# Performance work log

Hardware: AMD Instinct MI355X
Metric: run time of the kernel (lower is better)

The kernel has to match this reference:

```python
import jax, jax.numpy as jnp
import numpy as np

AZ = -999999.0  # ALMOST_ZERO_LOG_SCALE
N = 100000      # nodes
E = N - 1       # tree edges
D = 768         # input_dim
H = 256         # hidden_dim
C = 16          # num_classes


def setup_inputs() -> dict:
    key = jax.random.key(0)
    ks = jax.random.split(key, 14)
    scale = 0.02
    features = jax.random.normal(ks[0], (N, D), dtype=jnp.float32)
    # tree edges: child i (1..N-1) has parent sampled from [0, N)
    parent_idx = jax.random.randint(ks[1], (E,), 0, N, dtype=jnp.int32)
    child_idx = jnp.arange(1, N, dtype=jnp.int32)
    label_observed = jax.random.randint(ks[2], (N,), 0, 2, dtype=jnp.int32)
    true_labels = jax.random.randint(ks[3], (N,), 0, C, dtype=jnp.int32)
    # MLP feature extractor (num_layers=2, Linear+ReLU each, feature_extractor=True)
    W1 = jax.random.normal(ks[4], (D, H), dtype=jnp.float32) * scale
    b1 = jnp.zeros((H,), dtype=jnp.float32)
    W2 = jax.random.normal(ks[5], (H, H), dtype=jnp.float32) * scale
    b2 = jnp.zeros((H,), dtype=jnp.float32)
    # build_unary_potentials: Linear(H, C)
    Wu = jax.random.normal(ks[6], (H, C), dtype=jnp.float32) * scale
    bu = jnp.zeros((C,), dtype=jnp.float32)
    # build_edge_potentials: Linear(2H, C*C)
    We = jax.random.normal(ks[7], (2 * H, C * C), dtype=jnp.float32) * scale
    be = jnp.zeros((C * C,), dtype=jnp.float32)
    return {
        "features": features, "parent_idx": parent_idx, "child_idx": child_idx,
        "label_observed": label_observed, "true_labels": true_labels,
        "W1": W1, "b1": b1, "W2": W2, "b2": b2,
        "Wu": Wu, "bu": bu, "We": We, "be": be,
    }


def reference(features, parent_idx, child_idx, label_observed, true_labels,
              W1, b1, W2, b2, Wu, bu, We, be):
    obs = label_observed.astype(bool)
    # MLP feature extractor over all nodes at once (original loops per-node)
    h = jax.nn.relu(features @ W1 + b1)
    h = jax.nn.relu(h @ W2 + b2)                      # [N, H]
    # unary potentials; observed nodes get 0 at true label, AZ elsewhere
    unary_pred = h @ Wu + bu                          # [N, C]
    lbl = jnp.arange(C, dtype=true_labels.dtype)
    obs_unary = jnp.where(true_labels[:, None] == lbl[None, :], 0.0, AZ)
    unary = jnp.where(obs[:, None], obs_unary, unary_pred)  # [N, C]
    # edge potentials: Linear on concat(parent_hidden, child_hidden)
    hp = h[parent_idx]                                # [E, H]
    hc = h[child_idx]                                 # [E, H]
    ep = (jnp.concatenate([hp, hc], axis=1) @ We + be).reshape(E, C, C)
    pl = true_labels[parent_idx]                      # [E]
    cl = true_labels[child_idx]                       # [E]
    op = obs[parent_idx]                              # [E]
    oc = obs[child_idx]                               # [E]
    row = lbl[None, :, None]                          # broadcast over rows
    col = lbl[None, None, :]                          # broadcast over cols
    # both observed: 0 at [parent_label, child_label], AZ elsewhere
    allow_both = (row == pl[:, None, None]) & (col == cl[:, None, None])
    both = (op & oc)[:, None, None]
    # child-only observed: keep row at child label; parent-only: keep col at parent label
    keep = (((oc & ~op)[:, None, None] & (row == cl[:, None, None]))
            | ((op & ~oc)[:, None, None] & (col == pl[:, None, None]))
            | (~op & ~oc)[:, None, None])
    ep_masked = jnp.where(both,
                          jnp.where(allow_both, 0.0, AZ),
                          jnp.where(keep, ep, ep + AZ))
    return unary, ep_masked
```

## Files before the change

kernel.cpp:

```cpp
#include <hip/hip_runtime.h>
#include <cstddef>

#define AZ -999999.0f

typedef float  f32x4  __attribute__((ext_vector_type(4)));
typedef short  s16x8  __attribute__((ext_vector_type(8)));
typedef __bf16 bf16x8 __attribute__((ext_vector_type(8)));
typedef unsigned short ushort_t;

__device__ __forceinline__ ushort_t f2bf(float f) {
    return __builtin_bit_cast(ushort_t, (__bf16)f);
}

__device__ __forceinline__ f32x4 mfma16(s16x8 a, s16x8 b, f32x4 c) {
    return __builtin_amdgcn_mfma_f32_16x16x32_bf16(
        __builtin_bit_cast(bf16x8, a), __builtin_bit_cast(bf16x8, b), c, 0, 0, 0);
}

__device__ __forceinline__ void gl2lds16(const void* g, void* l) {
    __builtin_amdgcn_global_load_lds(
        (const __attribute__((address_space(1))) unsigned int*)g,
        (__attribute__((address_space(3))) unsigned int*)l, 16, 0, 0);
}

__global__ void setup_kernel(
    const float* __restrict__ W1, const float* __restrict__ W2,
    const float* __restrict__ We, const float* __restrict__ Wu,
    ushort_t* __restrict__ W1T, ushort_t* __restrict__ W2T,
    ushort_t* __restrict__ WeT, ushort_t* __restrict__ WuTs,
    const int* __restrict__ pidx, const int* __restrict__ cidx,
    const int* __restrict__ tl, const int* __restrict__ obs,
    int* __restrict__ meta, int E)
{
    int b = blockIdx.x, t = threadIdx.x;
    if (b < 768) {
        int idx = b * 256 + t; int k = idx >> 8, n = idx & 255;
        W1T[(size_t)n * 768 + k] = f2bf(W1[idx]);
    } else if (b < 1024) {
        int idx = (b - 768) * 256 + t; int k = idx >> 8, n = idx & 255;
        W2T[n * 256 + k] = f2bf(W2[idx]);
    } else if (b < 1536) {
        int idx = (b - 1024) * 256 + t; int k = idx >> 8, n = idx & 255;
        WeT[(size_t)n * 512 + k] = f2bf(We[idx]);
    } else if (b < 1552) {
        int idx = (b - 1536) * 256 + t; int k = idx >> 4, c = idx & 15;
        WuTs[c * 256 + (((k >> 3) ^ (c & 7)) << 3) + (k & 7)] = f2bf(Wu[idx]);
    } else {
        int e = (b - 1552) * 256 + t;
        if (e < E) {
            int p = pidx[e], c = cidx[e];
            meta[e] = (tl[p] & 15) | ((tl[c] & 15) << 4)
                    | ((obs[p] & 1) << 8) | ((obs[c] & 1) << 9);
        }
    }
}

__global__ __launch_bounds__(256) void node_fused_kernel(
    const float* __restrict__ features, const ushort_t* __restrict__ W1T,
    const float* __restrict__ b1, const ushort_t* __restrict__ W2T,
    const float* __restrict__ b2, const ushort_t* __restrict__ WuTs,
    const float* __restrict__ bu, const int* __restrict__ tl,
    const int* __restrict__ obs, ushort_t* __restrict__ h2,
    float* __restrict__ out_unary, int N)
{
    __shared__ __align__(16) char smem[65536];
    float*    Asf = (float*)smem;
    ushort_t* Bsh = (ushort_t*)(smem + 8192);
    ushort_t* Hsh = (ushort_t*)(smem + 24576);
    ushort_t* Wsh = (ushort_t*)(smem + 57344);

    const int tid = threadIdx.x, lane = tid & 63, wave = tid >> 6;
    const int quad = lane >> 4, l16 = lane & 15;
    const int row0 = blockIdx.x * 64;
    const int wc = wave * 64;

#pragma unroll
    for (int j = 0; j < 2; ++j)
        gl2lds16(WuTs + j * 2048 + wave * 512 + lane * 8,
                 (char*)Wsh + j * 4096 + wave * 1024);

    const int c4 = tid & 3, rB = tid >> 2;
    const int gcB = c4 ^ ((rB >> 1) & 3);
    unsigned lds_b[4];
#pragma unroll
    for (int j = 0; j < 4; ++j) lds_b[j] = (unsigned)(j * 64 + wave * 16) * 64;

    const int c8 = tid & 7, r8 = tid >> 3;
    const int gcA = c8 ^ (r8 & 7);
    size_t a_off[2]; unsigned lds_a[2];
#pragma unroll
    for (int j = 0; j < 2; ++j) {
        int gr = row0 + j * 32 + r8; if (gr > N - 1) gr = N - 1;
        a_off[j] = (size_t)gr * 768 + gcA * 4;
        lds_a[j] = (unsigned)(j * 32 + wave * 8) * 128;
    }

    const f32x4 fz = {0.f, 0.f, 0.f, 0.f};
    f32x4 acc[4][4];
#pragma unroll
    for (int i = 0; i < 4; ++i)
#pragma unroll
        for (int j = 0; j < 4; ++j) acc[i][j] = fz;

    for (int kt = 0; kt < 24; ++kt) {
        const int kbase = kt << 5;
#pragma unroll
        for (int j = 0; j < 2; ++j)
            gl2lds16(features + a_off[j] + kbase, smem + lds_a[j]);
#pragma unroll
        for (int j = 0; j < 4; ++j)
            gl2lds16(W1T + (size_t)(j * 64 + rB) * 768 + gcB * 8 + kbase,
                     (char*)Bsh + lds_b[j]);
        __syncthreads();

        s16x8 af[4], bf[4];
        const int s = l16 & 7;
        const int c0 = (2 * quad) ^ s, c1 = c0 ^ 1;
#pragma unroll
        for (int f = 0; f < 4; ++f) {
            int row = f * 16 + l16;
            f32x4 v0 = *(const f32x4*)&Asf[row * 32 + c0 * 4];
            f32x4 v1 = *(const f32x4*)&Asf[row * 32 + c1 * 4];
            s16x8 a;
            a[0] = (short)f2bf(v0[0]); a[1] = (short)f2bf(v0[1]);
            a[2] = (short)f2bf(v0[2]); a[3] = (short)f2bf(v0[3]);
            a[4] = (short)f2bf(v1[0]); a[5] = (short)f2bf(v1[1]);
            a[6] = (short)f2bf(v1[2]); a[7] = (short)f2bf(v1[3]);
            af[f] = a;
        }
        const int cb = quad ^ ((l16 >> 1) & 3);
#pragma unroll
        for (int f = 0; f < 4; ++f)
            bf[f] = *(const s16x8*)&Bsh[(wc + f * 16 + l16) * 32 + cb * 8];
#pragma unroll
        for (int fr = 0; fr < 4; ++fr)
#pragma unroll
            for (int fc = 0; fc < 4; ++fc)
                acc[fr][fc] = mfma16(af[fr], bf[fc], acc[fr][fc]);
        __syncthreads();
    }

    {
        float bv[4];
#pragma unroll
        for (int fc = 0; fc < 4; ++fc) bv[fc] = b1[wc + fc * 16 + l16];
#pragma unroll
        for (int fr = 0; fr < 4; ++fr) {
#pragma unroll
            for (int r = 0; r < 4; ++r) {
                int row = fr * 16 + quad * 4 + r;
#pragma unroll
                for (int fc = 0; fc < 4; ++fc) {
                    int col = wc + fc * 16 + l16;
                    float v = acc[fr][fc][r] + bv[fc];
                    v = v > 0.f ? v : 0.f;
                    Hsh[row * 256 + (((col >> 3) ^ (row & 7)) << 3) + (col & 7)] = f2bf(v);
                }
            }
        }
    }
#pragma unroll
    for (int i = 0; i < 4; ++i)
#pragma unroll
        for (int j = 0; j < 4; ++j) acc[i][j] = fz;

    for (int kt = 0; kt < 8; ++kt) {
        const int kbase = kt << 5;
#pragma unroll
        for (int j = 0; j < 4; ++j)
            gl2lds16(W2T + (size_t)(j * 64 + rB) * 256 + gcB * 8 + kbase,
                     (char*)Bsh + lds_b[j]);
        __syncthreads();

        s16x8 af[4], bf[4];
        const int pc = (kt * 4 + quad) ^ (l16 & 7);
#pragma unroll
        for (int f = 0; f < 4; ++f)
            af[f] = *(const s16x8*)&Hsh[(f * 16 + l16) * 256 + pc * 8];
        const int cb = quad ^ ((l16 >> 1) & 3);
#pragma unroll
        for (int f = 0; f < 4; ++f)
            bf[f] = *(const s16x8*)&Bsh[(wc + f * 16 + l16) * 32 + cb * 8];
#pragma unroll
        for (int fr = 0; fr < 4; ++fr)
#pragma unroll
            for (int fc = 0; fc < 4; ++fc)
                acc[fr][fc] = mfma16(af[fr], bf[fc], acc[fr][fc]);
        __syncthreads();
    }

    {
        float bv[4];
#pragma unroll
        for (int fc = 0; fc < 4; ++fc) bv[fc] = b2[wc + fc * 16 + l16];
#pragma unroll
        for (int fr = 0; fr < 4; ++fr) {
#pragma unroll
            for (int r = 0; r < 4; ++r) {
                int row = fr * 16 + quad * 4 + r;
#pragma unroll
                for (int fc = 0; fc < 4; ++fc) {
                    int col = wc + fc * 16 + l16;
                    float v = acc[fr][fc][r] + bv[fc];
                    v = v > 0.f ? v : 0.f;
                    Hsh[row * 256 + (((col >> 3) ^ (row & 7)) << 3) + (col & 7)] = f2bf(v);
                }
            }
        }
    }
    __syncthreads();

    {
        int row = tid >> 2, cc = tid & 3;
        int gr = row0 + row;
        if (gr < N) {
#pragma unroll
            for (int j = 0; j < 8; ++j) {
                int phys = (j * 4 + cc) ^ (row & 7);
                s16x8 v = *(const s16x8*)&Hsh[row * 256 + phys * 8];
                *(s16x8*)&h2[(size_t)gr * 256 + (j * 4 + cc) * 8] = v;
            }
        }
    }

    {
        const int arow = wave * 16 + l16;
        f32x4 accu = fz;
#pragma unroll
        for (int kt = 0; kt < 8; ++kt) {
            int pc = (kt * 4 + quad) ^ (l16 & 7);
            s16x8 a = *(const s16x8*)&Hsh[arow * 256 + pc * 8];
            s16x8 b = *(const s16x8*)&Wsh[l16 * 256 + pc * 8];
            accu = mfma16(a, b, accu);
        }
        float bvc = bu[l16];
#pragma unroll
        for (int r = 0; r < 4; ++r) {
            int node = row0 + wave * 16 + quad * 4 + r;
            if (node < N) {
                float v = obs[node] ? ((tl[node] == l16) ? 0.0f : AZ) : (accu[r] + bvc);
                out_unary[(size_t)node * 16 + l16] = v;
            }
        }
    }
}

__global__ __launch_bounds__(256) void edge_gemm_kernel(
    const ushort_t* __restrict__ h2, const ushort_t* __restrict__ WeT,
    const float* __restrict__ bias, float* __restrict__ out,
    int M,
    const int* __restrict__ parent_idx, const int* __restrict__ child_idx,
    const int* __restrict__ meta)
{
    __shared__ __align__(16) char smem[4096 + 16384];
    ushort_t* Ash = (ushort_t*)smem;
    ushort_t* Bsh = (ushort_t*)(smem + 4096);

    const int tid  = threadIdx.x;
    const int lane = tid & 63, wave = tid >> 6;
    const int row0 = blockIdx.x * 64;
    const int wc   = wave * 64;
    const int quad = lane >> 4, l16 = lane & 15;
    const int c4   = tid & 3, rB = tid >> 2;

    const int gcB = c4 ^ ((rB >> 1) & 3);
    size_t   b_off[4]; unsigned lds_b[4];
#pragma unroll
    for (int j = 0; j < 4; ++j) {
        b_off[j] = (size_t)(j * 64 + rB) * 512 + gcB * 8;
        lds_b[j] = (unsigned)(j * 64 + wave * 16) * 64;
    }

    int gr = row0 + rB; if (gr > M - 1) gr = M - 1;
    const int pn = parent_idx[gr], cn = child_idx[gr];
    const unsigned a_col  = (unsigned)gcB * 8;
    const unsigned lds_a0 = (unsigned)(wave * 16) * 64;

    const f32x4 fz = {0.f, 0.f, 0.f, 0.f};
    f32x4 acc[4][4];
#pragma unroll
    for (int i = 0; i < 4; ++i)
#pragma unroll
        for (int j = 0; j < 4; ++j) acc[i][j] = fz;

    for (int kt = 0; kt < 16; ++kt) {
        const int kbase = kt << 5;
        int node = (kbase < 256) ? pn : cn;
        gl2lds16(h2 + (size_t)node * 256 + (kbase & 255) + a_col, smem + lds_a0);
#pragma unroll
        for (int j = 0; j < 4; ++j)
            gl2lds16(WeT + b_off[j] + kbase, (char*)Bsh + lds_b[j]);

        __syncthreads();

        s16x8 af[4], bf[4];
        const int ca = quad ^ ((l16 >> 1) & 3);
#pragma unroll
        for (int f = 0; f < 4; ++f)
            af[f] = *(const s16x8*)&Ash[(f * 16 + l16) * 32 + ca * 8];
#pragma unroll
        for (int f = 0; f < 4; ++f)
            bf[f] = *(const s16x8*)&Bsh[(wc + f * 16 + l16) * 32 + ca * 8];
#pragma unroll
        for (int fr = 0; fr < 4; ++fr)
#pragma unroll
            for (int fc = 0; fc < 4; ++fc)
                acc[fr][fc] = mfma16(af[fr], bf[fc], acc[fr][fc]);
        __syncthreads();
    }

    float bv[4];
#pragma unroll
    for (int fc = 0; fc < 4; ++fc) bv[fc] = bias[wc + fc * 16 + l16];

#pragma unroll
    for (int fr = 0; fr < 4; ++fr) {
#pragma unroll
        for (int r = 0; r < 4; ++r) {
            int e = row0 + fr * 16 + quad * 4 + r;
            if (e < M) {
                int m  = meta[e];
                int pl = m & 15, cl = (m >> 4) & 15;
                int op = (m >> 8) & 1, oc = (m >> 9) & 1;
#pragma unroll
                for (int fc = 0; fc < 4; ++fc) {
                    int n = wc + fc * 16 + l16;
                    float v = acc[fr][fc][r] + bv[fc];
                    int rr = n >> 4, cc = n & 15;
                    if (op & oc)  v = (rr == pl && cc == cl) ? 0.0f : AZ;
                    else if (oc)  { if (rr != cl) v += AZ; }
                    else if (op)  { if (cc != pl) v += AZ; }
                    out[(size_t)e * 256 + n] = v;
                }
            }
        }
    }
}

extern "C" void kernel_launch(void* const* d_in, const int* in_sizes, int n_in,
                              void* d_out, int out_size, void* d_ws, size_t ws_size,
                              hipStream_t stream) {
    const float* features = (const float*)d_in[0];
    const int* parent_idx = (const int*)d_in[1];
    const int* child_idx  = (const int*)d_in[2];
    const int* label_obs  = (const int*)d_in[3];
    const int* true_lab   = (const int*)d_in[4];
    const float* W1 = (const float*)d_in[5];
    const float* b1 = (const float*)d_in[6];
    const float* W2 = (const float*)d_in[7];
    const float* b2 = (const float*)d_in[8];
    const float* Wu = (const float*)d_in[9];
    const float* bu = (const float*)d_in[10];
    const float* We = (const float*)d_in[11];
    const float* be = (const float*)d_in[12];
    float* out = (float*)d_out;

    const int N = 100000, E = N - 1;

    char* ws = (char*)d_ws;
    ushort_t* h2   = (ushort_t*)ws;
    ushort_t* W1T  = (ushort_t*)(ws + (size_t)N * 256 * 2);
    ushort_t* W2T  = W1T + 768 * 256;
    ushort_t* WeT  = W2T + 256 * 256;
    ushort_t* WuTs = WeT + 512 * 256;
    int*      meta = (int*)(WuTs + 16 * 256);

    setup_kernel<<<1943, 256, 0, stream>>>(W1, W2, We, Wu, W1T, W2T, WeT, WuTs,
                                           parent_idx, child_idx, true_lab, label_obs,
                                           meta, E);

    node_fused_kernel<<<(N + 63) / 64, 256, 0, stream>>>(
        features, W1T, b1, W2T, b2, WuTs, bu, true_lab, label_obs, h2, out, N);

    edge_gemm_kernel<<<(E + 63) / 64, 256, 0, stream>>>(
        h2, WeT, be, out + (size_t)N * 16, E, parent_idx, child_idx, meta);
}
```

Baseline: 608.7 us.

## Double-buffer LDS tiles in node and edge GEMM kernels with async prefetch

Converts the K-loops of the fused node MLP kernel and the edge GEMM kernel to double-buffered LDS staging. The next tile's global-to-LDS loads are issued before computing on the current tile, and manual vmcnt waits plus raw barriers replace the full __syncthreads. The W2 prefetch is chained into the tail of the W1 loop. The Wu tile is now read directly from global memory instead of being staged in LDS. This is meant to hide global load latency behind MFMA work, at the cost of more LDS per block (lower occupancy) and fragile hand-counted waitcnt values.

```diff
diff --git a/kernel.cpp b/kernel.cpp
--- a/kernel.cpp
+++ b/kernel.cpp
@@ -22,6 +22,8 @@
         (const __attribute__((address_space(1))) unsigned int*)g,
         (__attribute__((address_space(3))) unsigned int*)l, 16, 0, 0);
 }
+
+#define FENCE() asm volatile("" ::: "memory")
 
 __global__ void setup_kernel(
     const float* __restrict__ W1, const float* __restrict__ W2,
@@ -64,26 +66,21 @@
     float* __restrict__ out_unary, int N)
 {
     __shared__ __align__(16) char smem[65536];
-    float*    Asf = (float*)smem;
-    ushort_t* Bsh = (ushort_t*)(smem + 8192);
-    ushort_t* Hsh = (ushort_t*)(smem + 24576);
-    ushort_t* Wsh = (ushort_t*)(smem + 57344);
+    ushort_t* Hsh = (ushort_t*)(smem + 32768);
 
     const int tid = threadIdx.x, lane = tid & 63, wave = tid >> 6;
     const int quad = lane >> 4, l16 = lane & 15;
     const int row0 = blockIdx.x * 64;
     const int wc = wave * 64;
 
-#pragma unroll
-    for (int j = 0; j < 2; ++j)
-        gl2lds16(WuTs + j * 2048 + wave * 512 + lane * 8,
-                 (char*)Wsh + j * 4096 + wave * 1024);
-
     const int c4 = tid & 3, rB = tid >> 2;
     const int gcB = c4 ^ ((rB >> 1) & 3);
-    unsigned lds_b[4];
-#pragma unroll
-    for (int j = 0; j < 4; ++j) lds_b[j] = (unsigned)(j * 64 + wave * 16) * 64;
+    unsigned lds_b[4]; size_t b1_off[4];
+#pragma unroll
+    for (int j = 0; j < 4; ++j) {
+        lds_b[j]  = (unsigned)(j * 64 + wave * 16) * 64;
+        b1_off[j] = (size_t)(j * 64 + rB) * 768 + gcB * 8;
+    }
 
     const int c8 = tid & 7, r8 = tid >> 3;
     const int gcA = c8 ^ (r8 & 7);
@@ -102,17 +99,44 @@
 #pragma unroll
         for (int j = 0; j < 4; ++j) acc[i][j] = fz;
 
+    auto stageA = [&](int kt, int b) {
+        const int kbase = kt << 5;
+        char* Ab = smem + b * 8192;
+#pragma unroll
+        for (int j = 0; j < 2; ++j)
+            gl2lds16(features + a_off[j] + kbase, Ab + lds_a[j]);
+    };
+    auto stageB1 = [&](int kt, int b) {
+        const int kbase = kt << 5;
+        char* Bb = smem + 16384 + b * 16384;
+#pragma unroll
+        for (int j = 0; j < 4; ++j)
+            gl2lds16(W1T + b1_off[j] + kbase, Bb + lds_b[j]);
+    };
+    auto stageB2 = [&](int kt, int b) {
+        const int kbase = kt << 5;
+        char* Bb = smem + (b ? 0 : 16384);
+#pragma unroll
+        for (int j = 0; j < 4; ++j)
+            gl2lds16(W2T + (size_t)(j * 64 + rB) * 256 + gcB * 8 + kbase,
+                     Bb + lds_b[j]);
+    };
+
+    stageA(0, 0); stageB1(0, 0);
+    int cur = 0;
     for (int kt = 0; kt < 24; ++kt) {
-        const int kbase = kt << 5;
-#pragma unroll
-        for (int j = 0; j < 2; ++j)
-            gl2lds16(features + a_off[j] + kbase, smem + lds_a[j]);
-#pragma unroll
-        for (int j = 0; j < 4; ++j)
-            gl2lds16(W1T + (size_t)(j * 64 + rB) * 768 + gcB * 8 + kbase,
-                     (char*)Bsh + lds_b[j]);
-        __syncthreads();
-
+        if (kt < 23) {
+            stageA(kt + 1, cur ^ 1); stageB1(kt + 1, cur ^ 1);
+            asm volatile("s_waitcnt vmcnt(6)" ::: "memory");
+        } else {
+            stageB2(0, 0);
+            asm volatile("s_waitcnt vmcnt(4)" ::: "memory");
+        }
+        __builtin_amdgcn_s_barrier();
+        FENCE();
+
+        const float*    Asf = (const float*)(smem + cur * 8192);
+        const ushort_t* Bsh = (const ushort_t*)(smem + 16384 + cur * 16384);
         s16x8 af[4], bf[4];
         const int s = l16 & 7;
         const int c0 = (2 * quad) ^ s, c1 = c0 ^ 1;
@@ -137,7 +161,10 @@
 #pragma unroll
             for (int fc = 0; fc < 4; ++fc)
                 acc[fr][fc] = mfma16(af[fr], bf[fc], acc[fr][fc]);
-        __syncthreads();
+
+        FENCE();
+        __builtin_amdgcn_s_barrier();
+        cur ^= 1;
     }
 
     {
@@ -164,14 +191,22 @@
 #pragma unroll
         for (int j = 0; j < 4; ++j) acc[i][j] = fz;
 
+    asm volatile("s_waitcnt lgkmcnt(0)" ::: "memory");
+    __builtin_amdgcn_s_barrier();
+    FENCE();
+
+    int cur2 = 0;
     for (int kt = 0; kt < 8; ++kt) {
-        const int kbase = kt << 5;
-#pragma unroll
-        for (int j = 0; j < 4; ++j)
-            gl2lds16(W2T + (size_t)(j * 64 + rB) * 256 + gcB * 8 + kbase,
-                     (char*)Bsh + lds_b[j]);
-        __syncthreads();
-
+        if (kt < 7) {
+            stageB2(kt + 1, cur2 ^ 1);
+            asm volatile("s_waitcnt vmcnt(4)" ::: "memory");
+        } else {
+            asm volatile("s_waitcnt vmcnt(0)" ::: "memory");
+        }
+        __builtin_amdgcn_s_barrier();
+        FENCE();
+
+        const ushort_t* Bsh = (const ushort_t*)(smem + (cur2 ? 0 : 16384));
         s16x8 af[4], bf[4];
         const int pc = (kt * 4 + quad) ^ (l16 & 7);
 #pragma unroll
@@ -186,7 +221,10 @@
 #pragma unroll
             for (int fc = 0; fc < 4; ++fc)
                 acc[fr][fc] = mfma16(af[fr], bf[fc], acc[fr][fc]);
-        __syncthreads();
+
+        FENCE();
+        __builtin_amdgcn_s_barrier();
+        cur2 ^= 1;
     }
 
     {
@@ -208,7 +246,9 @@
             }
         }
     }
-    __syncthreads();
+    asm volatile("s_waitcnt lgkmcnt(0)" ::: "memory");
+    __builtin_amdgcn_s_barrier();
+    FENCE();
 
     {
         int row = tid >> 2, cc = tid & 3;
@@ -230,7 +270,7 @@
         for (int kt = 0; kt < 8; ++kt) {
             int pc = (kt * 4 + quad) ^ (l16 & 7);
             s16x8 a = *(const s16x8*)&Hsh[arow * 256 + pc * 8];
-            s16x8 b = *(const s16x8*)&Wsh[l16 * 256 + pc * 8];
+            s16x8 b = *(const s16x8*)&WuTs[l16 * 256 + pc * 8];
             accu = mfma16(a, b, accu);
         }
         float bvc = bu[l16];
@@ -252,9 +292,7 @@
     const int* __restrict__ parent_idx, const int* __restrict__ child_idx,
     const int* __restrict__ meta)
 {
-    __shared__ __align__(16) char smem[4096 + 16384];
-    ushort_t* Ash = (ushort_t*)smem;
-    ushort_t* Bsh = (ushort_t*)(smem + 4096);
+    __shared__ __align__(16) char smem[40960];
 
     const int tid  = threadIdx.x;
     const int lane = tid & 63, wave = tid >> 6;
@@ -276,6 +314,17 @@
     const unsigned a_col  = (unsigned)gcB * 8;
     const unsigned lds_a0 = (unsigned)(wave * 16) * 64;
 
+    auto stage = [&](int kt, int b) {
+        const int kbase = kt << 5;
+        int node = (kbase < 256) ? pn : cn;
+        gl2lds16(h2 + (size_t)node * 256 + (kbase & 255) + a_col,
+                 smem + b * 4096 + lds_a0);
+#pragma unroll
+        for (int j = 0; j < 4; ++j)
+            gl2lds16(WeT + b_off[j] + kbase,
+                     smem + 8192 + b * 16384 + lds_b[j]);
+    };
+
     const f32x4 fz = {0.f, 0.f, 0.f, 0.f};
     f32x4 acc[4][4];
 #pragma unroll
@@ -283,16 +332,20 @@
 #pragma unroll
         for (int j = 0; j < 4; ++j) acc[i][j] = fz;
 
+    stage(0, 0);
+    int cur = 0;
     for (int kt = 0; kt < 16; ++kt) {
-        const int kbase = kt << 5;
-        int node = (kbase < 256) ? pn : cn;
-        gl2lds16(h2 + (size_t)node * 256 + (kbase & 255) + a_col, smem + lds_a0);
-#pragma unroll
-        for (int j = 0; j < 4; ++j)
-            gl2lds16(WeT + b_off[j] + kbase, (char*)Bsh + lds_b[j]);
-
-        __syncthreads();
-
+        if (kt < 15) {
+            stage(kt + 1, cur ^ 1);
+            asm volatile("s_waitcnt vmcnt(5)" ::: "memory");
+        } else {
+            asm volatile("s_waitcnt vmcnt(0)" ::: "memory");
+        }
+        __builtin_amdgcn_s_barrier();
+        FENCE();
+
+        const ushort_t* Ash = (const ushort_t*)(smem + cur * 4096);
+        const ushort_t* Bsh = (const ushort_t*)(smem + 8192 + cur * 16384);
         s16x8 af[4], bf[4];
         const int ca = quad ^ ((l16 >> 1) & 3);
 #pragma unroll
@@ -306,7 +359,10 @@
 #pragma unroll
             for (int fc = 0; fc < 4; ++fc)
                 acc[fr][fc] = mfma16(af[fr], bf[fc], acc[fr][fc]);
-        __syncthreads();
+
+        FENCE();
+        __builtin_amdgcn_s_barrier();
+        cur ^= 1;
     }
 
     float bv[4];
```

Result: faster. 574.4 us (-5.6%).
